# Kernel tuning notes

Measured on AMD Instinct MI355X. Metric: run time of the kernel, lower is better.

## Reference

```python
import jax, jax.numpy as jnp
import numpy as np

K = 10          # neighbors, hard-coded in MLP1.forward
NEG_SLOPE = 0.2 # LeakyReLU slope
EPS = 1e-5      # BatchNorm2d default eps


def setup_inputs() -> dict:
    key = jax.random.key(0)
    k1, k2, k3, k4 = jax.random.split(key, 4)
    B, C, N = 8, 6, 4096
    x = jax.random.normal(k1, (B, C, N), dtype=jnp.float32)
    W = jax.random.normal(k2, (64, 6), dtype=jnp.float32) * 0.2      # conv1x1 weight (O, I)
    gamma = jax.random.uniform(k3, (64,), jnp.float32, 0.5, 1.5)     # BN weight
    beta = jax.random.normal(k4, (64,), dtype=jnp.float32) * 0.1     # BN bias
    return {"x": x, "W": W, "gamma": gamma, "beta": beta}


def _knn_idx(x3, k):
    # pairwise_distance[b,i,j] = -||x_i - x_j||^2 (as in the torch knn)
    inner = jnp.einsum('bdn,bdm->bnm', x3, x3)          # x_i . x_j
    xx = jnp.sum(x3 * x3, axis=1)                       # (B, N)
    pd = 2.0 * inner - xx[:, :, None] - xx[:, None, :]  # (B, N, N)
    _, idx = jax.lax.top_k(pd, k)                       # k nearest (incl. self)
    return idx                                          # (B, N, k) int32


def reference(x, W, gamma, beta):
    # x: (B, 6, N)
    idx = _knn_idx(x[:, :3], K)                          # (B, N, k)
    # gather neighbor features: feat[b,c,n,j] = x[b,c,idx[b,n,j]]
    feat = jax.vmap(lambda xb, ib: xb[:, ib])(x, idx)    # (B, 6, N, k)
    # center xyz over the k neighbors and scale by 10
    xyz = feat[:, :3]
    xyz = (xyz - jnp.mean(xyz, axis=-1, keepdims=True)) * 10.0
    feat = jnp.concatenate([xyz, feat[:, 3:]], axis=1)   # (B, 6, N, k)
    # 1x1 conv (6 -> 64), no bias
    y = jnp.einsum('oc,bcnk->bonk', W, feat)             # (B, 64, N, k)
    # BatchNorm2d in train mode: batch stats over (B, N, k), biased variance
    mu = jnp.mean(y, axis=(0, 2, 3), keepdims=True)
    var = jnp.mean((y - mu) ** 2, axis=(0, 2, 3), keepdims=True)
    y = (y - mu) * jax.lax.rsqrt(var + EPS)
    y = y * gamma[None, :, None, None] + beta[None, :, None, None]
    # LeakyReLU(0.2)
    y = jnp.where(y >= 0, y, NEG_SLOPE * y)
    # max over neighbors k
    y = jnp.max(y, axis=-1)                              # (B, 64, N)
    # global max + mean pooling over N, concat along last axis
    x1 = jnp.max(y, axis=-1)                             # (B, 64)
    x2 = jnp.mean(y, axis=-1)                            # (B, 64)
    return jnp.concatenate([x1, x2], axis=-1)            # (B, 128)
```

## Files before the change

kernel.cpp:

```cpp
#include <hip/hip_runtime.h>
#include <float.h>

#define K_NN 10
#define BATCH 8
#define CIN 6
#define NPTS 4096
#define COUT 64
#define NSEG 8
#define SEGLEN (NPTS / NSEG)
#define CHUNK 16
#define NCHUNK (SEGLEN / CHUNK)
#define NWORD (SEGLEN / 32)
#define NEG_SLOPE 0.2f
#define BN_EPS 1e-5f

static constexpr size_t OFF_PTS  = 0;
static constexpr size_t OFF_PTS2 = OFF_PTS + (size_t)BATCH * NPTS * sizeof(float4);
static constexpr size_t OFF_PTSP = OFF_PTS2 + (size_t)BATCH * NPTS * sizeof(float4);
static constexpr size_t OFF_Q    = OFF_PTSP + (size_t)BATCH * NPTS * sizeof(float4);
static constexpr size_t OFF_ST   = OFF_Q + (size_t)BATCH * COUT * NPTS * sizeof(float);

typedef float v2f __attribute__((ext_vector_type(2)));

__device__ __forceinline__ float wave_sum(float v) {
#pragma unroll
    for (int m = 32; m >= 1; m >>= 1) v += __shfl_xor(v, m, 64);
    return v;
}
__device__ __forceinline__ float wave_max(float v) {
#pragma unroll
    for (int m = 32; m >= 1; m >>= 1) v = fmaxf(v, __shfl_xor(v, m, 64));
    return v;
}

__device__ __forceinline__ float distp(float qx, float qy, float qz, float4 c) {
    return fmaf(c.x, qx, fmaf(c.y, qy, fmaf(c.z, qz, -c.w)));
}

__device__ __forceinline__ v2f dist2(v2f qx2, v2f qy2, v2f qz2, float4 fa, float4 fb) {
    v2f cx = {fa.x, fa.y}, cy = {fa.z, fa.w}, cz = {fb.x, fb.y}, cw = {fb.z, fb.w};
#if __has_builtin(__builtin_elementwise_fma)
    v2f t = __builtin_elementwise_fma(cz, qz2, -cw);
    t = __builtin_elementwise_fma(cy, qy2, t);
    t = __builtin_elementwise_fma(cx, qx2, t);
    return t;
#else
    v2f t;
    t[0] = fmaf(cx[0], qx2[0], fmaf(cy[0], qy2[0], fmaf(cz[0], qz2[0], -cw[0])));
    t[1] = fmaf(cx[1], qx2[1], fmaf(cy[1], qy2[1], fmaf(cz[1], qz2[1], -cw[1])));
    return t;
#endif
}

__device__ __forceinline__ v2f vmax2(v2f a, v2f b) {
#if __has_builtin(__builtin_elementwise_max)
    return __builtin_elementwise_max(a, b);
#else
    v2f r; r[0] = fmaxf(a[0], b[0]); r[1] = fmaxf(a[1], b[1]); return r;
#endif
}

#define CHL(cj) { float _hi = fmaxf(cj, t); t = fminf(cj, t); cj = _hi; }

#define CSWP(va, vb, ia, ib) \
    if (va > vb) { float _tv = va; va = vb; vb = _tv; int _ti = ia; ia = ib; ib = _ti; }

#define INSERT10(dd, mm) \
    if ((dd) > v9) { \
        v9 = (dd); i9 = (mm); \
        CSWP(v9, v8, i9, i8) \
        CSWP(v8, v7, i8, i7) \
        CSWP(v7, v6, i7, i6) \
        CSWP(v6, v5, i6, i5) \
        CSWP(v5, v4, i5, i4) \
        CSWP(v4, v3, i4, i3) \
        CSWP(v3, v2, i3, i2) \
        CSWP(v2, v1, i2, i1) \
        CSWP(v1, v0, i1, i0) \
    }

__global__ __launch_bounds__(256) void prep_pts(const float* __restrict__ x,
                                                float4* __restrict__ pts,
                                                float4* __restrict__ pts2,
                                                float4* __restrict__ ptsp,
                                                double* __restrict__ stats) {
    if (blockIdx.x == 0 && threadIdx.x < 27) stats[threadIdx.x] = 0.0;
    int t = blockIdx.x * 256 + threadIdx.x;
    int b = t >> 12;
    int n = t & (NPTS - 1);
    const float* xb = x + (size_t)b * CIN * NPTS;
    float X = xb[n];
    float Y = xb[NPTS + n];
    float Z = xb[2 * NPTS + n];
    float w = X * X + Y * Y + Z * Z;
    pts[t] = make_float4(2.0f * X, 2.0f * Y, 2.0f * Z, w);
    float x3 = xb[3 * NPTS + n];
    float x4 = xb[4 * NPTS + n];
    float x5 = xb[5 * NPTS + n];
    pts2[t] = make_float4(x3, x4, x5, 0.0f);
    float Xn = __shfl_down(X, 1, 64);
    float Yn = __shfl_down(Y, 1, 64);
    float Zn = __shfl_down(Z, 1, 64);
    float wn = __shfl_down(w, 1, 64);
    if ((n & 1) == 0) {
        float4* pb = ptsp + (size_t)b * NPTS;
        pb[n]     = make_float4(2.0f * X, 2.0f * Xn, 2.0f * Y, 2.0f * Yn);
        pb[n + 1] = make_float4(2.0f * Z, 2.0f * Zn, w, wn);
    }
}

__global__ __launch_bounds__(512, 4) void knnmf_kernel(const float4* __restrict__ pts,
                                                       const float4* __restrict__ pts2,
                                                       const float4* __restrict__ ptsp,
                                                       const float* __restrict__ W,
                                                       float* __restrict__ q,
                                                       double* __restrict__ stats) {
    __shared__ alignas(16) char smem[NSEG * SEGLEN * sizeof(float4)];
    __shared__ unsigned short idxL[K_NN][64];
    __shared__ float sW[COUT * CIN];
    __shared__ float sstat[27];

    for (int i = threadIdx.x; i < COUT * CIN; i += 512) sW[i] = W[i];

    int b  = blockIdx.y;
    int ln = threadIdx.x & 63;
    int wv = threadIdx.x >> 6;
    int wvu = __builtin_amdgcn_readfirstlane(wv);
    int n  = blockIdx.x * 64 + ln;
    const float4* p   = pts  + (size_t)b * NPTS;
    const float4* p2s = ptsp + (size_t)b * NPTS;
    float4 q4 = p[n];
    float qx = 0.5f * q4.x, qy = 0.5f * q4.y, qz = 0.5f * q4.z;
    v2f qx2 = {qx, qx}, qy2 = {qy, qy}, qz2 = {qz, qz};
    int m0 = wvu * SEGLEN;

    float4* slice = (float4*)(smem + (size_t)wvu * (SEGLEN * sizeof(float4)));

    {
        const float4* src = p2s + m0;
#pragma unroll
        for (int i = 0; i < SEGLEN / 64; i++)
            slice[ln + 64 * i] = src[ln + 64 * i];
    }

    {
        float c0 = -FLT_MAX, c1 = -FLT_MAX, c2 = -FLT_MAX, c3 = -FLT_MAX, c4 = -FLT_MAX;
        float c5 = -FLT_MAX, c6 = -FLT_MAX, c7 = -FLT_MAX, c8 = -FLT_MAX, c9 = -FLT_MAX;

        for (int ch = 0; ch < NCHUNK; ch++) {
            const float4* cp = slice + ch * CHUNK;
            v2f e0 = dist2(qx2, qy2, qz2, cp[0],  cp[1]);
            v2f e1 = dist2(qx2, qy2, qz2, cp[2],  cp[3]);
            v2f e2 = dist2(qx2, qy2, qz2, cp[4],  cp[5]);
            v2f e3 = dist2(qx2, qy2, qz2, cp[6],  cp[7]);
            v2f e4 = dist2(qx2, qy2, qz2, cp[8],  cp[9]);
            v2f e5 = dist2(qx2, qy2, qz2, cp[10], cp[11]);
            v2f e6 = dist2(qx2, qy2, qz2, cp[12], cp[13]);
            v2f e7 = dist2(qx2, qy2, qz2, cp[14], cp[15]);
            v2f a0 = vmax2(e0, e1);
            v2f a1 = vmax2(e2, e3);
            v2f a2 = vmax2(e4, e5);
            v2f a3 = vmax2(e6, e7);
            v2f b0 = vmax2(a0, a1);
            v2f b1 = vmax2(a2, a3);
            v2f cm = vmax2(b0, b1);
            float t = fmaxf(cm[0], cm[1]);
            CHL(c0) CHL(c1) CHL(c2) CHL(c3) CHL(c4)
            CHL(c5) CHL(c6) CHL(c7) CHL(c8) CHL(c9)
        }
        float thr = c9;

        float v0 = -FLT_MAX, v1 = -FLT_MAX, v2 = -FLT_MAX, v3 = -FLT_MAX, v4 = -FLT_MAX;
        float v5 = -FLT_MAX, v6 = -FLT_MAX, v7 = -FLT_MAX, v8 = -FLT_MAX, v9 = -FLT_MAX;
        int i0 = 0, i1 = 0, i2 = 0, i3 = 0, i4 = 0;
        int i5 = 0, i6 = 0, i7 = 0, i8 = 0, i9 = 0;

        for (int w = 0; w < NWORD; w++) {
            const float4* cp = slice + w * 32;
            unsigned int mask = 0u;
#pragma unroll
            for (int pr = 0; pr < 16; pr++) {
                v2f d2v = dist2(qx2, qy2, qz2, cp[2 * pr], cp[2 * pr + 1]);
                mask = (mask << 2) | (d2v[0] >= thr ? 2u : 0u) | (d2v[1] >= thr ? 1u : 0u);
            }
            int base = m0 + w * 32;
            while (mask) {
                int j = __builtin_clz(mask);
                mask ^= (0x80000000u >> j);
                int m = base + j;
                float4 cc = p[m];
                float d = distp(qx, qy, qz, cc);
                INSERT10(d, m)
            }
        }

        float* dpub = (float*)slice;
        unsigned short* ipub = (unsigned short*)((char*)slice + K_NN * 64 * sizeof(float));
        dpub[0 * 64 + ln] = v0; ipub[0 * 64 + ln] = (unsigned short)i0;
        dpub[1 * 64 + ln] = v1; ipub[1 * 64 + ln] = (unsigned short)i1;
        dpub[2 * 64 + ln] = v2; ipub[2 * 64 + ln] = (unsigned short)i2;
        dpub[3 * 64 + ln] = v3; ipub[3 * 64 + ln] = (unsigned short)i3;
        dpub[4 * 64 + ln] = v4; ipub[4 * 64 + ln] = (unsigned short)i4;
        dpub[5 * 64 + ln] = v5; ipub[5 * 64 + ln] = (unsigned short)i5;
        dpub[6 * 64 + ln] = v6; ipub[6 * 64 + ln] = (unsigned short)i6;
        dpub[7 * 64 + ln] = v7; ipub[7 * 64 + ln] = (unsigned short)i7;
        dpub[8 * 64 + ln] = v8; ipub[8 * 64 + ln] = (unsigned short)i8;
        dpub[9 * 64 + ln] = v9; ipub[9 * 64 + ln] = (unsigned short)i9;
    }
    __syncthreads();

    if (wvu == 0) {
        float v0 = -FLT_MAX, v1 = -FLT_MAX, v2 = -FLT_MAX, v3 = -FLT_MAX, v4 = -FLT_MAX;
        float v5 = -FLT_MAX, v6 = -FLT_MAX, v7 = -FLT_MAX, v8 = -FLT_MAX, v9 = -FLT_MAX;
        int i0 = 0, i1 = 0, i2 = 0, i3 = 0, i4 = 0;
        int i5 = 0, i6 = 0, i7 = 0, i8 = 0, i9 = 0;
#pragma unroll
        for (int w = 0; w < NSEG; w++) {
            const float* dp = (const float*)(smem + (size_t)w * (SEGLEN * sizeof(float4)));
            const unsigned short* ip = (const unsigned short*)((const char*)dp + K_NN * 64 * sizeof(float));
#pragma unroll
            for (int j = 0; j < K_NN; j++) {
                float d = dp[j * 64 + ln];
                int m = ip[j * 64 + ln];
                INSERT10(d, m)
            }
        }
        idxL[0][ln] = (unsigned short)i0;
        idxL[1][ln] = (unsigned short)i1;
        idxL[2][ln] = (unsigned short)i2;
        idxL[3][ln] = (unsigned short)i3;
        idxL[4][ln] = (unsigned short)i4;
        idxL[5][ln] = (unsigned short)i5;
        idxL[6][ln] = (unsigned short)i6;
        idxL[7][ln] = (unsigned short)i7;
        idxL[8][ln] = (unsigned short)i8;
        idxL[9][ln] = (unsigned short)i9;
    }
    __syncthreads();

    const float4* p2 = pts2 + (size_t)b * NPTS;

    int nb[K_NN];
#pragma unroll
    for (int k = 0; k < K_NN; k++) nb[k] = idxL[k][ln];

    float f[CIN][K_NN];
#pragma unroll
    for (int k = 0; k < K_NN; k++) {
        float4 c = p[nb[k]];
        f[0][k] = 0.5f * c.x; f[1][k] = 0.5f * c.y; f[2][k] = 0.5f * c.z;
    }
#pragma unroll
    for (int k = 0; k < K_NN; k++) {
        float4 c2 = p2[nb[k]];
        f[3][k] = c2.x; f[4][k] = c2.y; f[5][k] = c2.z;
    }

#pragma unroll
    for (int c = 0; c < 3; c++) {
        float s = 0.f;
#pragma unroll
        for (int k = 0; k < K_NN; k++) s += f[c][k];
        float m = s / 10.0f;
#pragma unroll
        for (int k = 0; k < K_NN; k++) f[c][k] = (f[c][k] - m) * 10.0f;
    }

    float* qb = q + (size_t)b * COUT * NPTS + n;
    int o0 = wvu * 8;
#pragma unroll
    for (int oo = 0; oo < 8; oo++) {
        int o = o0 + oo;
        float w0 = sW[o * 6 + 0], w1 = sW[o * 6 + 1], w2 = sW[o * 6 + 2];
        float w3 = sW[o * 6 + 3], w4 = sW[o * 6 + 4], w5 = sW[o * 6 + 5];
        float mx = -FLT_MAX;
#pragma unroll
        for (int k = 0; k < K_NN; k++) {
            float y = w0 * f[0][k] + w1 * f[1][k] + w2 * f[2][k] +
                      w3 * f[3][k] + w4 * f[4][k] + w5 * f[5][k];
            mx = fmaxf(mx, y);
        }
        qb[(size_t)o * NPTS] = mx;
    }

    if (wvu == 0) {
        float s1[CIN];
#pragma unroll
        for (int c = 0; c < CIN; c++) {
            float s = 0.f;
#pragma unroll
            for (int k = 0; k < K_NN; k++) s += f[c][k];
            s1[c] = s;
        }
        float s2[21];
#pragma unroll
        for (int i = 0; i < 21; i++) s2[i] = 0.f;
#pragma unroll
        for (int k = 0; k < K_NN; k++) {
            int pp = 0;
#pragma unroll
            for (int c = 0; c < CIN; c++)
#pragma unroll
                for (int c2 = c; c2 < CIN; c2++) {
                    s2[pp] += f[c][k] * f[c2][k];
                    pp++;
                }
        }
#pragma unroll
        for (int c = 0; c < CIN; c++) s1[c] = wave_sum(s1[c]);
#pragma unroll
        for (int i = 0; i < 21; i++) s2[i] = wave_sum(s2[i]);

        if (ln == 0) {
#pragma unroll
            for (int c = 0; c < CIN; c++) sstat[c] = s1[c];
#pragma unroll
            for (int i = 0; i < 21; i++) sstat[6 + i] = s2[i];
        }
        if (ln < 27) atomicAdd(&stats[ln], (double)sstat[ln]);
    }
}

__global__ __launch_bounds__(256) void reduce_kernel(const float* __restrict__ q,
                                                     const double* __restrict__ stats,
                                                     const float* __restrict__ W,
                                                     const float* __restrict__ gamma,
                                                     const float* __restrict__ beta,
                                                     float* __restrict__ out) {
    int o = blockIdx.x;
    int b = blockIdx.y;

    __shared__ float s_sc, s_sh;
    if (threadIdx.x == 0) {
        const double minv = 1.0 / (double)((size_t)BATCH * NPTS * K_NN);
        double w[CIN];
#pragma unroll
        for (int c = 0; c < CIN; c++) w[c] = (double)W[o * CIN + c];
        double mu = 0.0;
#pragma unroll
        for (int c = 0; c < CIN; c++) mu += w[c] * stats[c];
        mu *= minv;
        double ey2 = 0.0;
        int pp = 6;
#pragma unroll
        for (int c = 0; c < CIN; c++)
#pragma unroll
            for (int c2 = c; c2 < CIN; c2++) {
                double v = w[c] * w[c2] * stats[pp];
                ey2 += (c2 == c) ? v : 2.0 * v;
                pp++;
            }
        ey2 *= minv;
        double var = ey2 - mu * mu;
        float scale = gamma[o] * rsqrtf((float)var + BN_EPS);
        float shift = beta[o] - (float)mu * scale;
        s_sc = scale;
        s_sh = shift;
    }
    __syncthreads();
    float scale = s_sc, shift = s_sh;

    const float* qp = q + ((size_t)b * COUT + o) * NPTS;
    float mx = -FLT_MAX, sm = 0.f;
    for (int i = threadIdx.x; i < NPTS; i += 256) {
        float z = scale * qp[i] + shift;
        z = (z >= 0.f) ? z : NEG_SLOPE * z;
        mx = fmaxf(mx, z);
        sm += z;
    }
    mx = wave_max(mx);
    sm = wave_sum(sm);
    __shared__ float smx[4], ssm2[4];
    int wv = threadIdx.x >> 6;
    int ln = threadIdx.x & 63;
    if (ln == 0) { smx[wv] = mx; ssm2[wv] = sm; }
    __syncthreads();
    if (threadIdx.x == 0) {
        float m = fmaxf(fmaxf(smx[0], smx[1]), fmaxf(smx[2], smx[3]));
        float s = ssm2[0] + ssm2[1] + ssm2[2] + ssm2[3];
        out[b * 2 * COUT + o] = m;
        out[b * 2 * COUT + COUT + o] = s * (1.0f / (float)NPTS);
    }
}

extern "C" void kernel_launch(void* const* d_in, const int* in_sizes, int n_in,
                              void* d_out, int out_size, void* d_ws, size_t ws_size,
                              hipStream_t stream) {
    const float* x     = (const float*)d_in[0];
    const float* W     = (const float*)d_in[1];
    const float* gamma = (const float*)d_in[2];
    const float* beta  = (const float*)d_in[3];
    float* out = (float*)d_out;

    char* ws = (char*)d_ws;
    float4* pts   = (float4*)(ws + OFF_PTS);
    float4* pts2  = (float4*)(ws + OFF_PTS2);
    float4* ptsp  = (float4*)(ws + OFF_PTSP);
    float*  q     = (float*)(ws + OFF_Q);
    double* stats = (double*)(ws + OFF_ST);

    prep_pts<<<BATCH * NPTS / 256, 256, 0, stream>>>(x, pts, pts2, ptsp, stats);
    knnmf_kernel<<<dim3(NPTS / 64, BATCH), 512, 0, stream>>>(pts, pts2, ptsp, W, q, stats);
    reduce_kernel<<<dim3(COUT, BATCH), 256, 0, stream>>>(q, stats, W, gamma, beta, out);
}
```

Before: 163.4 us.

## Fuse prep, kNN and reduce into one cooperative kernel with grid syncs

Merges the three launches into a single cooperative kernel: the first wave of each block does point preparation, a grid-wide sync follows, then the kNN and conv-statistics phase, another grid sync, and finally the BN/LeakyReLU/pool reduction with one block per (channel, batch). The aim is to remove launch gaps and inter-kernel drain between the three stages. The cost is two grid barriers and a requirement that all 512 blocks are co-resident. If the cooperative launch fails, the original three-kernel path runs as a fallback.

```diff
diff --git a/kernel.cpp b/kernel.cpp
--- a/kernel.cpp
+++ b/kernel.cpp
@@ -1,5 +1,8 @@
 #include <hip/hip_runtime.h>
+#include <hip/hip_cooperative_groups.h>
 #include <float.h>
+
+namespace cg = cooperative_groups;
 
 #define K_NN 10
 #define BATCH 8
@@ -79,54 +82,18 @@
         CSWP(v1, v0, i1, i0) \
     }
 
-__global__ __launch_bounds__(256) void prep_pts(const float* __restrict__ x,
-                                                float4* __restrict__ pts,
-                                                float4* __restrict__ pts2,
-                                                float4* __restrict__ ptsp,
-                                                double* __restrict__ stats) {
-    if (blockIdx.x == 0 && threadIdx.x < 27) stats[threadIdx.x] = 0.0;
-    int t = blockIdx.x * 256 + threadIdx.x;
-    int b = t >> 12;
-    int n = t & (NPTS - 1);
-    const float* xb = x + (size_t)b * CIN * NPTS;
-    float X = xb[n];
-    float Y = xb[NPTS + n];
-    float Z = xb[2 * NPTS + n];
-    float w = X * X + Y * Y + Z * Z;
-    pts[t] = make_float4(2.0f * X, 2.0f * Y, 2.0f * Z, w);
-    float x3 = xb[3 * NPTS + n];
-    float x4 = xb[4 * NPTS + n];
-    float x5 = xb[5 * NPTS + n];
-    pts2[t] = make_float4(x3, x4, x5, 0.0f);
-    float Xn = __shfl_down(X, 1, 64);
-    float Yn = __shfl_down(Y, 1, 64);
-    float Zn = __shfl_down(Z, 1, 64);
-    float wn = __shfl_down(w, 1, 64);
-    if ((n & 1) == 0) {
-        float4* pb = ptsp + (size_t)b * NPTS;
-        pb[n]     = make_float4(2.0f * X, 2.0f * Xn, 2.0f * Y, 2.0f * Yn);
-        pb[n + 1] = make_float4(2.0f * Z, 2.0f * Zn, w, wn);
-    }
-}
-
-__global__ __launch_bounds__(512, 4) void knnmf_kernel(const float4* __restrict__ pts,
-                                                       const float4* __restrict__ pts2,
-                                                       const float4* __restrict__ ptsp,
-                                                       const float* __restrict__ W,
-                                                       float* __restrict__ q,
-                                                       double* __restrict__ stats) {
-    __shared__ alignas(16) char smem[NSEG * SEGLEN * sizeof(float4)];
-    __shared__ unsigned short idxL[K_NN][64];
-    __shared__ float sW[COUT * CIN];
-    __shared__ float sstat[27];
-
+__device__ __forceinline__ void knnmf_phases(char* smem,
+                                             unsigned short (*idxL)[64],
+                                             float* sW, float* sstat,
+                                             const float4* __restrict__ pts,
+                                             const float4* __restrict__ pts2,
+                                             const float4* __restrict__ ptsp,
+                                             const float* __restrict__ W,
+                                             float* __restrict__ q,
+                                             double* __restrict__ stats,
+                                             int b, int ln, int wv, int wvu, int n) {
     for (int i = threadIdx.x; i < COUT * CIN; i += 512) sW[i] = W[i];
 
-    int b  = blockIdx.y;
-    int ln = threadIdx.x & 63;
-    int wv = threadIdx.x >> 6;
-    int wvu = __builtin_amdgcn_readfirstlane(wv);
-    int n  = blockIdx.x * 64 + ln;
     const float4* p   = pts  + (size_t)b * NPTS;
     const float4* p2s = ptsp + (size_t)b * NPTS;
     float4 q4 = p[n];
@@ -321,16 +288,60 @@
     }
 }
 
-__global__ __launch_bounds__(256) void reduce_kernel(const float* __restrict__ q,
-                                                     const double* __restrict__ stats,
-                                                     const float* __restrict__ W,
-                                                     const float* __restrict__ gamma,
-                                                     const float* __restrict__ beta,
-                                                     float* __restrict__ out) {
-    int o = blockIdx.x;
-    int b = blockIdx.y;
-
-    __shared__ float s_sc, s_sh;
+__global__ __launch_bounds__(512, 4) void fused_all(const float* __restrict__ x,
+                                                    const float* __restrict__ W,
+                                                    const float* __restrict__ gamma,
+                                                    const float* __restrict__ beta,
+                                                    float4* __restrict__ pts,
+                                                    float4* __restrict__ pts2,
+                                                    float4* __restrict__ ptsp,
+                                                    float* __restrict__ q,
+                                                    double* __restrict__ stats,
+                                                    float* __restrict__ out) {
+    __shared__ alignas(16) char smem[NSEG * SEGLEN * sizeof(float4)];
+    __shared__ unsigned short idxL[K_NN][64];
+    __shared__ float sW[COUT * CIN];
+    __shared__ float sstat[27];
+    __shared__ float s_sc, s_sh, smx[4], ssm2[4];
+
+    cg::grid_group gg = cg::this_grid();
+
+    int b  = blockIdx.y;
+    int bx = blockIdx.x;
+    int ln = threadIdx.x & 63;
+    int wv = threadIdx.x >> 6;
+    int wvu = __builtin_amdgcn_readfirstlane(wv);
+    int n  = bx * 64 + ln;
+
+    if (bx == 0 && b == 0 && threadIdx.x < 27) stats[threadIdx.x] = 0.0;
+    if (wvu == 0) {
+        int t = b * NPTS + n;
+        const float* xb = x + (size_t)b * CIN * NPTS;
+        float X = xb[n];
+        float Y = xb[NPTS + n];
+        float Z = xb[2 * NPTS + n];
+        float w = X * X + Y * Y + Z * Z;
+        pts[t] = make_float4(2.0f * X, 2.0f * Y, 2.0f * Z, w);
+        pts2[t] = make_float4(xb[3 * NPTS + n], xb[4 * NPTS + n], xb[5 * NPTS + n], 0.0f);
+        float Xn = __shfl_down(X, 1, 64);
+        float Yn = __shfl_down(Y, 1, 64);
+        float Zn = __shfl_down(Z, 1, 64);
+        float wn = __shfl_down(w, 1, 64);
+        if ((n & 1) == 0) {
+            float4* pb = ptsp + (size_t)b * NPTS;
+            pb[n]     = make_float4(2.0f * X, 2.0f * Xn, 2.0f * Y, 2.0f * Yn);
+            pb[n + 1] = make_float4(2.0f * Z, 2.0f * Zn, w, wn);
+        }
+    }
+    __threadfence();
+    gg.sync();
+
+    knnmf_phases(smem, idxL, sW, sstat, pts, pts2, ptsp, W, q, stats, b, ln, wv, wvu, n);
+
+    __threadfence();
+    gg.sync();
+
+    int o = bx;
     if (threadIdx.x == 0) {
         const double minv = 1.0 / (double)((size_t)BATCH * NPTS * K_NN);
         double w[CIN];
@@ -360,6 +371,110 @@
     __syncthreads();
     float scale = s_sc, shift = s_sh;
 
+    const float* qp = q + ((size_t)b * COUT + o) * NPTS;
+    float mx = -FLT_MAX, sm = 0.f;
+    if (threadIdx.x < 256) {
+        for (int i = threadIdx.x; i < NPTS; i += 256) {
+            float z = scale * qp[i] + shift;
+            z = (z >= 0.f) ? z : NEG_SLOPE * z;
+            mx = fmaxf(mx, z);
+            sm += z;
+        }
+        mx = wave_max(mx);
+        sm = wave_sum(sm);
+        if (ln == 0) { smx[wv] = mx; ssm2[wv] = sm; }
+    }
+    __syncthreads();
+    if (threadIdx.x == 0) {
+        float m = fmaxf(fmaxf(smx[0], smx[1]), fmaxf(smx[2], smx[3]));
+        float s = ssm2[0] + ssm2[1] + ssm2[2] + ssm2[3];
+        out[b * 2 * COUT + o] = m;
+        out[b * 2 * COUT + COUT + o] = s * (1.0f / (float)NPTS);
+    }
+}
+
+__global__ __launch_bounds__(256) void prep_pts(const float* __restrict__ x,
+                                                float4* __restrict__ pts,
+                                                float4* __restrict__ pts2,
+                                                float4* __restrict__ ptsp,
+                                                double* __restrict__ stats) {
+    if (blockIdx.x == 0 && threadIdx.x < 27) stats[threadIdx.x] = 0.0;
+    int t = blockIdx.x * 256 + threadIdx.x;
+    int b = t >> 12;
+    int n = t & (NPTS - 1);
+    const float* xb = x + (size_t)b * CIN * NPTS;
+    float X = xb[n];
+    float Y = xb[NPTS + n];
+    float Z = xb[2 * NPTS + n];
+    float w = X * X + Y * Y + Z * Z;
+    pts[t] = make_float4(2.0f * X, 2.0f * Y, 2.0f * Z, w);
+    pts2[t] = make_float4(xb[3 * NPTS + n], xb[4 * NPTS + n], xb[5 * NPTS + n], 0.0f);
+    float Xn = __shfl_down(X, 1, 64);
+    float Yn = __shfl_down(Y, 1, 64);
+    float Zn = __shfl_down(Z, 1, 64);
+    float wn = __shfl_down(w, 1, 64);
+    if ((n & 1) == 0) {
+        float4* pb = ptsp + (size_t)b * NPTS;
+        pb[n]     = make_float4(2.0f * X, 2.0f * Xn, 2.0f * Y, 2.0f * Yn);
+        pb[n + 1] = make_float4(2.0f * Z, 2.0f * Zn, w, wn);
+    }
+}
+
+__global__ __launch_bounds__(512, 4) void knnmf_kernel(const float4* __restrict__ pts,
+                                                       const float4* __restrict__ pts2,
+                                                       const float4* __restrict__ ptsp,
+                                                       const float* __restrict__ W,
+                                                       float* __restrict__ q,
+                                                       double* __restrict__ stats) {
+    __shared__ alignas(16) char smem[NSEG * SEGLEN * sizeof(float4)];
+    __shared__ unsigned short idxL[K_NN][64];
+    __shared__ float sW[COUT * CIN];
+    __shared__ float sstat[27];
+    int b  = blockIdx.y;
+    int ln = threadIdx.x & 63;
+    int wv = threadIdx.x >> 6;
+    int wvu = __builtin_amdgcn_readfirstlane(wv);
+    int n  = blockIdx.x * 64 + ln;
+    knnmf_phases(smem, idxL, sW, sstat, pts, pts2, ptsp, W, q, stats, b, ln, wv, wvu, n);
+}
+
+__global__ __launch_bounds__(256) void reduce_kernel(const float* __restrict__ q,
+                                                     const double* __restrict__ stats,
+                                                     const float* __restrict__ W,
+                                                     const float* __restrict__ gamma,
+                                                     const float* __restrict__ beta,
+                                                     float* __restrict__ out) {
+    int o = blockIdx.x;
+    int b = blockIdx.y;
+    __shared__ float s_sc, s_sh;
+    if (threadIdx.x == 0) {
+        const double minv = 1.0 / (double)((size_t)BATCH * NPTS * K_NN);
+        double w[CIN];
+#pragma unroll
+        for (int c = 0; c < CIN; c++) w[c] = (double)W[o * CIN + c];
+        double mu = 0.0;
+#pragma unroll
+        for (int c = 0; c < CIN; c++) mu += w[c] * stats[c];
+        mu *= minv;
+        double ey2 = 0.0;
+        int pp = 6;
+#pragma unroll
+        for (int c = 0; c < CIN; c++)
+#pragma unroll
+            for (int c2 = c; c2 < CIN; c2++) {
+                double v = w[c] * w[c2] * stats[pp];
+                ey2 += (c2 == c) ? v : 2.0 * v;
+                pp++;
+            }
+        ey2 *= minv;
+        double var = ey2 - mu * mu;
+        float scale = gamma[o] * rsqrtf((float)var + BN_EPS);
+        float shift = beta[o] - (float)mu * scale;
+        s_sc = scale;
+        s_sh = shift;
+    }
+    __syncthreads();
+    float scale = s_sc, shift = s_sh;
     const float* qp = q + ((size_t)b * COUT + o) * NPTS;
     float mx = -FLT_MAX, sm = 0.f;
     for (int i = threadIdx.x; i < NPTS; i += 256) {
@@ -399,7 +514,15 @@
     float*  q     = (float*)(ws + OFF_Q);
     double* stats = (double*)(ws + OFF_ST);
 
-    prep_pts<<<BATCH * NPTS / 256, 256, 0, stream>>>(x, pts, pts2, ptsp, stats);
-    knnmf_kernel<<<dim3(NPTS / 64, BATCH), 512, 0, stream>>>(pts, pts2, ptsp, W, q, stats);
-    reduce_kernel<<<dim3(COUT, BATCH), 256, 0, stream>>>(q, stats, W, gamma, beta, out);
-}
+    void* args[] = {(void*)&x, (void*)&W, (void*)&gamma, (void*)&beta,
+                    (void*)&pts, (void*)&pts2, (void*)&ptsp,
+                    (void*)&q, (void*)&stats, (void*)&out};
+    hipError_t err = hipLaunchCooperativeKernel((const void*)fused_all,
+                                                dim3(NPTS / 64, BATCH), dim3(512),
+                                                args, 0, stream);
+    if (err != hipSuccess) {
+        prep_pts<<<BATCH * NPTS / 256, 256, 0, stream>>>(x, pts, pts2, ptsp, stats);
+        knnmf_kernel<<<dim3(NPTS / 64, BATCH), 512, 0, stream>>>(pts, pts2, ptsp, W, q, stats);
+        reduce_kernel<<<dim3(COUT, BATCH), 256, 0, stream>>>(q, stats, W, gamma, beta, out);
+    }
+}
```

Measured after the change: 420.2 us. 157% more time.

## Fuse point preprocessing into kNN kernel and replace stats atomics with partials

Applied to the files above, without the earlier changes.

Removes the prep_pts kernel. The kNN kernel now reads raw x directly, builds the paired xyz/norm layout in shared memory itself, and refines candidates from shared memory instead of global pts. The neighbor gather reads the six channels from x. Double atomics on the BN statistics are replaced by per-block partial sums, and reduce_kernel re-reduces these partials in every block. This saves one launch and the intermediate buffers, at the cost of redundant partial reduction and strided gathers.

```diff
diff --git a/kernel.cpp b/kernel.cpp
--- a/kernel.cpp
+++ b/kernel.cpp
@@ -14,11 +14,8 @@
 #define NEG_SLOPE 0.2f
 #define BN_EPS 1e-5f
 
-static constexpr size_t OFF_PTS  = 0;
-static constexpr size_t OFF_PTS2 = OFF_PTS + (size_t)BATCH * NPTS * sizeof(float4);
-static constexpr size_t OFF_PTSP = OFF_PTS2 + (size_t)BATCH * NPTS * sizeof(float4);
-static constexpr size_t OFF_Q    = OFF_PTSP + (size_t)BATCH * NPTS * sizeof(float4);
-static constexpr size_t OFF_ST   = OFF_Q + (size_t)BATCH * COUT * NPTS * sizeof(float);
+static constexpr size_t OFF_Q  = 0;
+static constexpr size_t OFF_SP = OFF_Q + (size_t)BATCH * COUT * NPTS * sizeof(float);
 
 typedef float v2f __attribute__((ext_vector_type(2)));
 
@@ -79,42 +76,10 @@
         CSWP(v1, v0, i1, i0) \
     }
 
-__global__ __launch_bounds__(256) void prep_pts(const float* __restrict__ x,
-                                                float4* __restrict__ pts,
-                                                float4* __restrict__ pts2,
-                                                float4* __restrict__ ptsp,
-                                                double* __restrict__ stats) {
-    if (blockIdx.x == 0 && threadIdx.x < 27) stats[threadIdx.x] = 0.0;
-    int t = blockIdx.x * 256 + threadIdx.x;
-    int b = t >> 12;
-    int n = t & (NPTS - 1);
-    const float* xb = x + (size_t)b * CIN * NPTS;
-    float X = xb[n];
-    float Y = xb[NPTS + n];
-    float Z = xb[2 * NPTS + n];
-    float w = X * X + Y * Y + Z * Z;
-    pts[t] = make_float4(2.0f * X, 2.0f * Y, 2.0f * Z, w);
-    float x3 = xb[3 * NPTS + n];
-    float x4 = xb[4 * NPTS + n];
-    float x5 = xb[5 * NPTS + n];
-    pts2[t] = make_float4(x3, x4, x5, 0.0f);
-    float Xn = __shfl_down(X, 1, 64);
-    float Yn = __shfl_down(Y, 1, 64);
-    float Zn = __shfl_down(Z, 1, 64);
-    float wn = __shfl_down(w, 1, 64);
-    if ((n & 1) == 0) {
-        float4* pb = ptsp + (size_t)b * NPTS;
-        pb[n]     = make_float4(2.0f * X, 2.0f * Xn, 2.0f * Y, 2.0f * Yn);
-        pb[n + 1] = make_float4(2.0f * Z, 2.0f * Zn, w, wn);
-    }
-}
-
-__global__ __launch_bounds__(512, 4) void knnmf_kernel(const float4* __restrict__ pts,
-                                                       const float4* __restrict__ pts2,
-                                                       const float4* __restrict__ ptsp,
+__global__ __launch_bounds__(512, 4) void knnmf_kernel(const float* __restrict__ x,
                                                        const float* __restrict__ W,
                                                        float* __restrict__ q,
-                                                       double* __restrict__ stats) {
+                                                       double* __restrict__ spart) {
     __shared__ alignas(16) char smem[NSEG * SEGLEN * sizeof(float4)];
     __shared__ unsigned short idxL[K_NN][64];
     __shared__ float sW[COUT * CIN];
@@ -123,24 +88,34 @@
     for (int i = threadIdx.x; i < COUT * CIN; i += 512) sW[i] = W[i];
 
     int b  = blockIdx.y;
+    int bx = blockIdx.x;
     int ln = threadIdx.x & 63;
     int wv = threadIdx.x >> 6;
     int wvu = __builtin_amdgcn_readfirstlane(wv);
-    int n  = blockIdx.x * 64 + ln;
-    const float4* p   = pts  + (size_t)b * NPTS;
-    const float4* p2s = ptsp + (size_t)b * NPTS;
-    float4 q4 = p[n];
-    float qx = 0.5f * q4.x, qy = 0.5f * q4.y, qz = 0.5f * q4.z;
+    int n  = bx * 64 + ln;
+    const float* xb = x + (size_t)b * CIN * NPTS;
+
+    float qx = xb[n];
+    float qy = xb[NPTS + n];
+    float qz = xb[2 * NPTS + n];
     v2f qx2 = {qx, qx}, qy2 = {qy, qy}, qz2 = {qz, qz};
     int m0 = wvu * SEGLEN;
 
     float4* slice = (float4*)(smem + (size_t)wvu * (SEGLEN * sizeof(float4)));
 
     {
-        const float4* src = p2s + m0;
-#pragma unroll
-        for (int i = 0; i < SEGLEN / 64; i++)
-            slice[ln + 64 * i] = src[ln + 64 * i];
+        const float2* sx = (const float2*)(xb + m0);
+        const float2* sy = (const float2*)(xb + NPTS + m0);
+        const float2* sz = (const float2*)(xb + 2 * NPTS + m0);
+#pragma unroll
+        for (int j = 0; j < SEGLEN / 2 / 64; j++) {
+            int pr = ln + 64 * j;
+            float2 X = sx[pr], Y = sy[pr], Z = sz[pr];
+            float w0 = X.x * X.x + Y.x * Y.x + Z.x * Z.x;
+            float w1 = X.y * X.y + Y.y * Y.y + Z.y * Z.y;
+            slice[2 * pr]     = make_float4(2.0f * X.x, 2.0f * X.y, 2.0f * Y.x, 2.0f * Y.y);
+            slice[2 * pr + 1] = make_float4(2.0f * Z.x, 2.0f * Z.y, w0, w1);
+        }
     }
 
     {
@@ -183,14 +158,17 @@
                 v2f d2v = dist2(qx2, qy2, qz2, cp[2 * pr], cp[2 * pr + 1]);
                 mask = (mask << 2) | (d2v[0] >= thr ? 2u : 0u) | (d2v[1] >= thr ? 1u : 0u);
             }
-            int base = m0 + w * 32;
+            int base = w * 32;
             while (mask) {
                 int j = __builtin_clz(mask);
                 mask ^= (0x80000000u >> j);
-                int m = base + j;
-                float4 cc = p[m];
+                int li = base + j;
+                float4 fa = slice[2 * (li >> 1)];
+                float4 fb = slice[2 * (li >> 1) + 1];
+                float4 cc = (li & 1) ? make_float4(fa.y, fa.w, fb.y, fb.w)
+                                     : make_float4(fa.x, fa.z, fb.x, fb.z);
                 float d = distp(qx, qy, qz, cc);
-                INSERT10(d, m)
+                INSERT10(d, m0 + li)
             }
         }
 
@@ -238,8 +216,6 @@
     }
     __syncthreads();
 
-    const float4* p2 = pts2 + (size_t)b * NPTS;
-
     int nb[K_NN];
 #pragma unroll
     for (int k = 0; k < K_NN; k++) nb[k] = idxL[k][ln];
@@ -247,13 +223,12 @@
     float f[CIN][K_NN];
 #pragma unroll
     for (int k = 0; k < K_NN; k++) {
-        float4 c = p[nb[k]];
-        f[0][k] = 0.5f * c.x; f[1][k] = 0.5f * c.y; f[2][k] = 0.5f * c.z;
-    }
-#pragma unroll
-    for (int k = 0; k < K_NN; k++) {
-        float4 c2 = p2[nb[k]];
-        f[3][k] = c2.x; f[4][k] = c2.y; f[5][k] = c2.z;
+        f[0][k] = xb[nb[k]];
+        f[1][k] = xb[NPTS + nb[k]];
+        f[2][k] = xb[2 * NPTS + nb[k]];
+        f[3][k] = xb[3 * NPTS + nb[k]];
+        f[4][k] = xb[4 * NPTS + nb[k]];
+        f[5][k] = xb[5 * NPTS + nb[k]];
     }
 
 #pragma unroll
@@ -317,18 +292,36 @@
 #pragma unroll
             for (int i = 0; i < 21; i++) sstat[6 + i] = s2[i];
         }
-        if (ln < 27) atomicAdd(&stats[ln], (double)sstat[ln]);
+        int blk = b * (NPTS / 64) + bx;
+        if (ln < 27) spart[(size_t)blk * 32 + ln] = (double)sstat[ln];
     }
 }
 
 __global__ __launch_bounds__(256) void reduce_kernel(const float* __restrict__ q,
-                                                     const double* __restrict__ stats,
+                                                     const double* __restrict__ spart,
                                                      const float* __restrict__ W,
                                                      const float* __restrict__ gamma,
                                                      const float* __restrict__ beta,
                                                      float* __restrict__ out) {
     int o = blockIdx.x;
     int b = blockIdx.y;
+    int wv = threadIdx.x >> 6;
+    int ln = threadIdx.x & 63;
+
+    __shared__ double sred[4][27];
+    __shared__ double sstatd[27];
+    if (ln < 27) {
+        double acc = 0.0;
+        int b0 = wv * 128;
+        for (int blk = b0; blk < b0 + 128; blk++)
+            acc += spart[(size_t)blk * 32 + ln];
+        sred[wv][ln] = acc;
+    }
+    __syncthreads();
+    if (threadIdx.x < 27)
+        sstatd[threadIdx.x] = sred[0][threadIdx.x] + sred[1][threadIdx.x] +
+                              sred[2][threadIdx.x] + sred[3][threadIdx.x];
+    __syncthreads();
 
     __shared__ float s_sc, s_sh;
     if (threadIdx.x == 0) {
@@ -338,7 +331,7 @@
         for (int c = 0; c < CIN; c++) w[c] = (double)W[o * CIN + c];
         double mu = 0.0;
 #pragma unroll
-        for (int c = 0; c < CIN; c++) mu += w[c] * stats[c];
+        for (int c = 0; c < CIN; c++) mu += w[c] * sstatd[c];
         mu *= minv;
         double ey2 = 0.0;
         int pp = 6;
@@ -346,7 +339,7 @@
         for (int c = 0; c < CIN; c++)
 #pragma unroll
             for (int c2 = c; c2 < CIN; c2++) {
-                double v = w[c] * w[c2] * stats[pp];
+                double v = w[c] * w[c2] * sstatd[pp];
                 ey2 += (c2 == c) ? v : 2.0 * v;
                 pp++;
             }
@@ -371,8 +364,6 @@
     mx = wave_max(mx);
     sm = wave_sum(sm);
     __shared__ float smx[4], ssm2[4];
-    int wv = threadIdx.x >> 6;
-    int ln = threadIdx.x & 63;
     if (ln == 0) { smx[wv] = mx; ssm2[wv] = sm; }
     __syncthreads();
     if (threadIdx.x == 0) {
@@ -393,13 +384,9 @@
     float* out = (float*)d_out;
 
     char* ws = (char*)d_ws;
-    float4* pts   = (float4*)(ws + OFF_PTS);
-    float4* pts2  = (float4*)(ws + OFF_PTS2);
-    float4* ptsp  = (float4*)(ws + OFF_PTSP);
     float*  q     = (float*)(ws + OFF_Q);
-    double* stats = (double*)(ws + OFF_ST);
-
-    prep_pts<<<BATCH * NPTS / 256, 256, 0, stream>>>(x, pts, pts2, ptsp, stats);
-    knnmf_kernel<<<dim3(NPTS / 64, BATCH), 512, 0, stream>>>(pts, pts2, ptsp, W, q, stats);
-    reduce_kernel<<<dim3(COUT, BATCH), 256, 0, stream>>>(q, stats, W, gamma, beta, out);
-}
+    double* spart = (double*)(ws + OFF_SP);
+
+    knnmf_kernel<<<dim3(NPTS / 64, BATCH), 512, 0, stream>>>(x, W, q, spart);
+    reduce_kernel<<<dim3(COUT, BATCH), 256, 0, stream>>>(q, spart, W, gamma, beta, out);
+}
```

Measured after the change: 172.4 us. 1.06x slower.
